# Performance work log

Measured on AMD Instinct MI355X. Metric: run time of the kernel, lower is better.

The kernel has to match this reference:

```python
import jax, jax.numpy as jnp
import numpy as np

N_LAYERS = 24
HID = 512
HEADS = 16
HEAD_DIM = HID // HEADS
CAP = 2048
VOCAB = 1025
EOS = 1024
FF = 2048
PE_LEN = 4096
EPS = 1e-5


def setup_inputs() -> dict:
    key = jax.random.key(0)
    ks = jax.random.split(key, 24)
    g = lambda k, shp, s=0.05: jax.random.normal(k, shp, jnp.float32) * s
    return {
        'last_token': jax.random.randint(ks[0], (1, 1), 0, 1024, dtype=jnp.int32),
        'position_index': jax.random.randint(ks[1], (1,), 0, 1024, dtype=jnp.int32),
        'cache_len': jax.random.randint(ks[2], (1,), 0, 1024, dtype=jnp.int32),
        'k_cache': g(ks[3], (N_LAYERS, 1, CAP, HID)),
        'v_cache': g(ks[4], (N_LAYERS, 1, CAP, HID)),
        'emb_table': g(ks[5], (VOCAB, HID)),
        'pe_table': g(ks[6], (PE_LEN, HID)),
        'x_scale': jnp.ones((1,), jnp.float32),
        'alpha': jnp.ones((1,), jnp.float32),
        'qkv_w_t': g(ks[7], (N_LAYERS, HID, 3 * HID)),
        'qkv_b': g(ks[8], (N_LAYERS, 3 * HID)),
        'out_w_t': g(ks[9], (N_LAYERS, HID, HID)),
        'out_b': g(ks[10], (N_LAYERS, HID)),
        'norm_w1': jnp.ones((N_LAYERS, HID), jnp.float32),
        'norm_b1': jnp.zeros((N_LAYERS, HID), jnp.float32),
        'norm_w2': jnp.ones((N_LAYERS, HID), jnp.float32),
        'norm_b2': jnp.zeros((N_LAYERS, HID), jnp.float32),
        'w1_t': g(ks[11], (N_LAYERS, HID, FF)),
        'b1': g(ks[12], (N_LAYERS, FF)),
        'w2_t': g(ks[13], (N_LAYERS, FF, HID)),
        'b2': g(ks[14], (N_LAYERS, HID)),
        'pred_w': g(ks[15], (VOCAB, HID)),
        'pred_b': g(ks[16], (VOCAB,)),
    }


def _layer_norm(x, w, b):
    mu = jnp.mean(x, axis=-1, keepdims=True)
    var = jnp.mean((x - mu) ** 2, axis=-1, keepdims=True)
    return (x - mu) * jax.lax.rsqrt(var + EPS) * w + b


def _decode_core(xy, cache_len, k_cache, v_cache, qkv_w_t, qkv_b, out_w_t, out_b,
                 norm_w1, norm_b1, norm_w2, norm_b2, w1_t, b1, w2_t, b2):
    B, Q, _ = xy.shape  # [1, 1, HID]
    clen = cache_len.astype(jnp.int32).reshape(1)
    next_len = clen + Q
    positions = jnp.arange(CAP)
    write_mask = (positions == clen)[None, :, None]           # [1, CAP, 1]
    valid = (positions < next_len)[None, :, None]             # [1, CAP, 1]
    inv_attn = (positions >= next_len)[None, None, None, :]   # [1, 1, 1, CAP]

    def layer(x, p):
        qw, qb, ow, ob, nw1, nb1, nw2, nb2, W1, B1, W2, B2, kc, vc = p
        qkv = x @ qw + qb                       # [B, Q, 3*HID]
        q, k, v = jnp.split(qkv, 3, axis=-1)
        # one-hot slot write + zero invalid tail (faithful to _update_cache_slot/_zero_invalid_cache_tail)
        kc = jnp.where(valid, jnp.where(write_mask, k, kc), 0.0)
        vc = jnp.where(valid, jnp.where(write_mask, v, vc), 0.0)
        qh = q.reshape(B, Q, HEADS, HEAD_DIM).transpose(0, 2, 1, 3)
        kh = kc.reshape(B, CAP, HEADS, HEAD_DIM).transpose(0, 2, 1, 3)
        vh = vc.reshape(B, CAP, HEADS, HEAD_DIM).transpose(0, 2, 1, 3)
        scores = jnp.einsum('bhqd,bhkd->bhqk', qh, kh) / jnp.sqrt(jnp.float32(HEAD_DIM))
        scores = jnp.where(inv_attn, jnp.float32(-1e30), scores)
        attn = jax.nn.softmax(scores, axis=-1)
        o = jnp.einsum('bhqk,bhkd->bhqd', attn, vh).transpose(0, 2, 1, 3).reshape(B, Q, HID)
        o = o @ ow + ob
        x = _layer_norm(x + o, nw1, nb1)
        h = jax.nn.relu(x @ W1 + B1) @ W2 + B2
        x = _layer_norm(x + h, nw2, nb2)
        return x, (kc, vc)

    x, (k_out, v_out) = jax.lax.scan(
        layer, xy,
        (qkv_w_t, qkv_b, out_w_t, out_b, norm_w1, norm_b1, norm_w2, norm_b2,
         w1_t, b1, w2_t, b2, k_cache, v_cache))
    return x, k_out, v_out, next_len


def reference(last_token, position_index, cache_len, k_cache, v_cache,
              emb_table, pe_table, x_scale, alpha,
              qkv_w_t, qkv_b, out_w_t, out_b,
              norm_w1, norm_b1, norm_w2, norm_b2,
              w1_t, b1, w2_t, b2, pred_w, pred_b):
    y_emb = emb_table[last_token]                              # [B, Q, HID]
    pos = pe_table[position_index.astype(jnp.int32)][None]     # [1, Q, HID]
    xy = y_emb * x_scale[0] + alpha[0] * pos
    x, k_out, v_out, next_len = _decode_core(
        xy, cache_len, k_cache, v_cache, qkv_w_t, qkv_b, out_w_t, out_b,
        norm_w1, norm_b1, norm_w2, norm_b2, w1_t, b1, w2_t, b2)
    logits = x[:, -1] @ pred_w.T + pred_b                      # [B, VOCAB]
    sampled = jnp.argmax(logits, axis=-1, keepdims=True).astype(jnp.int32)
    eos = (sampled.reshape(-1) == EOS).astype(jnp.int32)
    next_pos = position_index.astype(jnp.int32).reshape(1) + 1
    return (logits, sampled, eos, next_len, next_pos, k_out, v_out)
```

## Files before the change

### kernel.cpp

```cpp
#include <hip/hip_runtime.h>
#include <math.h>

#define NL     24
#define HIDDEN 512
#define H3     1536
#define HD     32
#define CAPCTX 2048
#define FFD    2048
#define NVOCAB 1025
#define GRID   256
#define NT     256
#define EPSLN  1e-5f
#define ISQ    0.17677669529663687f

__device__ __forceinline__ float gld(const float* p){ return __hip_atomic_load(p, __ATOMIC_RELAXED, __HIP_MEMORY_SCOPE_AGENT); }
__device__ __forceinline__ void  gst(float* p, float v){ __hip_atomic_store(p, v, __ATOMIC_RELAXED, __HIP_MEMORY_SCOPE_AGENT); }
__device__ __forceinline__ int   ild(const int* p){ return __hip_atomic_load(p, __ATOMIC_RELAXED, __HIP_MEMORY_SCOPE_AGENT); }
__device__ __forceinline__ void  ist(int* p, int v){ __hip_atomic_store(p, v, __ATOMIC_RELAXED, __HIP_MEMORY_SCOPE_AGENT); }

__device__ __forceinline__ void done_add(int* ctr, int tid){
  __syncthreads();
  if (tid == 0) __hip_atomic_fetch_add(ctr, 1, __ATOMIC_RELAXED, __HIP_MEMORY_SCOPE_AGENT);
}
__device__ __forceinline__ void waitge1(const int* c, int tgt){
  if (threadIdx.x == 0){
    int g = 0;
    while (__hip_atomic_load(c, __ATOMIC_RELAXED, __HIP_MEMORY_SCOPE_AGENT) < tgt){
      if (++g > (1<<25)) break;
    }
  }
  __syncthreads();
}
__device__ __forceinline__ void waitgeN(const int* base, int n, int tgt){
  if ((int)threadIdx.x < n){
    const int* c = base + threadIdx.x*16;
    int g = 0;
    while (__hip_atomic_load(c, __ATOMIC_RELAXED, __HIP_MEMORY_SCOPE_AGENT) < tgt){
      if (++g > (1<<25)) break;
    }
  }
  __syncthreads();
}
#define PIN() asm volatile("" ::: "memory")

#define KVF(kb)   ((kb)*16)
#define HEADC(h)  ((64+(h))*16)
#define FF1G(g)   ((80+(g))*16)
#define PRED_C    (88*16)
#define SLINE(par,h) ((90 + (par)*16 + (h))*16)

struct LdsF { float xn[HIDDEN]; float red[16*17]; float r8[8]; float s16[16]; float h16[16]; };
struct LdsAt{ float xn[HIDDEN]; float q[HD]; float e[128]; float v[128*33]; float red[288]; float r8[8]; float o32[HD]; };
union  Lds  { LdsF f; LdsAt a; };

__device__ __forceinline__ void bsum2(float &a, float &bb, float* lds8, int tid){
  #pragma unroll
  for (int o=32;o;o>>=1){ a += __shfl_down(a,o); bb += __shfl_down(bb,o); }
  __syncthreads();
  if ((tid&63)==0){ int w=tid>>6; lds8[w]=a; lds8[4+w]=bb; }
  __syncthreads();
  a  = lds8[0]+lds8[1]+lds8[2]+lds8[3];
  bb = lds8[4]+lds8[5]+lds8[6]+lds8[7];
  __syncthreads();
}

template<int K>
__device__ __forceinline__ float dotred(const float* w, const float* xn, float* red, int tid){
  const int c = tid & 15, s = tid >> 4;
  float a = 0.f;
  #pragma unroll
  for (int k=0;k<K;k++) a += xn[s + 16*k] * w[k];
  red[s*17 + c] = a;
  __syncthreads();
  float d = 0.f;
  if (s == 0){
    #pragma unroll
    for (int k=0;k<16;k++) d += red[k*17 + c];
  }
  __syncthreads();
  return d;
}

__device__ __forceinline__ void kvcopy(int idx, int T, int l, int clen,
    const float* __restrict__ KC, const float* __restrict__ VC,
    float* KO, float* VO, int tid){
  const int t7 = tid & 127, halfr = tid >> 7;
  const float4 z4 = make_float4(0.f,0.f,0.f,0.f);
  for (int r0 = idx*2; r0 < 4096; r0 += 2*T){
    int r = r0 + halfr;
    int p = r & 2047, isv = r >> 11;
    if (p != clen){
      float4* dst = (float4*)((isv ? VO : KO) + ((size_t)l*CAPCTX + p)*HIDDEN);
      if (p < clen){
        const float4* src = (const float4*)((isv ? VC : KC) + ((size_t)l*CAPCTX + p)*HIDDEN);
        dst[t7] = src[t7];
      } else {
        dst[t7] = z4;
      }
    }
  }
}

__global__ __launch_bounds__(NT, 1)
void t2s_decode(const int* __restrict__ LT, const int* __restrict__ PI, const int* __restrict__ CL,
                const float* __restrict__ KC, const float* __restrict__ VC,
                const float* __restrict__ EMB, const float* __restrict__ PE,
                const float* __restrict__ XSc, const float* __restrict__ ALp,
                const float* __restrict__ QKVW, const float* __restrict__ QKVB,
                const float* __restrict__ OUTW, const float* __restrict__ OUTB,
                const float* __restrict__ NW1, const float* __restrict__ NB1,
                const float* __restrict__ NW2, const float* __restrict__ NB2,
                const float* __restrict__ W1, const float* __restrict__ B1,
                const float* __restrict__ W2, const float* __restrict__ B2,
                const float* __restrict__ PW, const float* __restrict__ PB,
                float* __restrict__ OUT, float* __restrict__ WS)
{
  __shared__ Lds L;
  const int b = blockIdx.x, tid = threadIdx.x;

  int* C = (int*)WS;
  float* F   = WS + 2048;
  float* wop = F;
  float* wf2 = F + 16384;
  float* wx  = F + 24576;
  float* wx1 = F + 25088;
  float* wkv = F + 25600;

  float* KO = OUT + 1029;
  float* VO = KO + (size_t)NL*CAPCTX*HIDDEN;

  const int token = LT[0], posi = PI[0], clen = CL[0], nlen = clen + 1;
  const int nch = (nlen + 127) >> 7;
  const int T_copy = 128 + 16*(8 - nch);

  if (b >= 128){
    const int t = b - 128, h = t & 15, ci = t >> 4;
    const int cstar = clen >> 7;

    if (ci >= nch){
      const int idx = 128 + (ci - nch)*16 + h;
      for (int l=0;l<NL;l++) kvcopy(idx, T_copy, l, clen, KC, VC, KO, VO, tid);
    } else {
      const int c = tid & 31, s5 = tid >> 5;
      const int pl = tid >> 1, half = tid & 1, dbase = half << 4;
      const int p = (ci << 7) + pl;
      const bool validp = (p < nlen);
      const bool isnew  = validp && (p == clen);

      for (int l=0;l<NL;l++){
        const int par = l & 1;
        float pfQ[64];
        {
          const float* Wq = QKVW + (size_t)l*HIDDEN*H3 + (size_t)s5*H3 + h*HD + c;
          #pragma unroll
          for (int k=0;k<64;k++) pfQ[k] = Wq[(size_t)(k*8)*H3];
        }
        float qb = QKVB[(size_t)l*H3 + h*HD + c];
        float pfO[64];
        {
          const float* Wo = OUTW + (size_t)l*HIDDEN*HIDDEN + (size_t)(h*HD)*HIDDEN + tid;
          #pragma unroll
          for (int d=0;d<32;d++){ pfO[d] = Wo[(size_t)d*HIDDEN]; pfO[32+d] = Wo[(size_t)d*HIDDEN + 256]; }
        }
        float kbuf[16], vbuf[16];
        if (validp && !isnew){
          const size_t rowoff = ((size_t)l*CAPCTX + p)*HIDDEN + h*HD + dbase;
          const float4* sk = (const float4*)(KC + rowoff);
          const float4* sv = (const float4*)(VC + rowoff);
          #pragma unroll
          for (int k4=0;k4<4;k4++){
            float4 a = sk[k4];
            kbuf[4*k4]=a.x; kbuf[4*k4+1]=a.y; kbuf[4*k4+2]=a.z; kbuf[4*k4+3]=a.w;
            float4 cc = sv[k4];
            vbuf[4*k4]=cc.x; vbuf[4*k4+1]=cc.y; vbuf[4*k4+2]=cc.z; vbuf[4*k4+3]=cc.w;
          }
        }
        float lnb[2]={0,0}, lnw[2]={0,0}, lnn[2]={0,0};
        if (l > 0){
          #pragma unroll
          for (int r=0;r<2;r++){
            int i = tid + r*NT;
            lnb[r] = B2[(size_t)(l-1)*HIDDEN + i];
            lnw[r] = NW2[(size_t)(l-1)*HIDDEN + i];
            lnn[r] = NB2[(size_t)(l-1)*HIDDEN + i];
          }
        }
        PIN();

        if (l > 0) waitgeN(C + FF1G(0), 8, 16*l);

        float xn0, xn1;
        if (l == 0){
          float xs = XSc[0], al = ALp[0];
          xn0 = EMB[(size_t)token*HIDDEN + tid]*xs       + al*PE[(size_t)posi*HIDDEN + tid];
          xn1 = EMB[(size_t)token*HIDDEN + tid + 256]*xs + al*PE[(size_t)posi*HIDDEN + tid + 256];
        } else {
          float t0 = gld(&wx1[tid]) + lnb[0];
          float t1 = gld(&wx1[tid+256]) + lnb[1];
          const float* f2p = wf2 + (par^1)*4096;
          #pragma unroll
          for (int rg=0; rg<8; rg++){
            t0 += gld(&f2p[rg*512 + tid]);
            t1 += gld(&f2p[rg*512 + tid + 256]);
          }
          float s1 = t0 + t1, s2 = t0*t0 + t1*t1;
          bsum2(s1, s2, L.a.r8, tid);
          float mu = s1*(1.f/HIDDEN), rstd = rsqrtf(s2*(1.f/HIDDEN)-mu*mu+EPSLN);
          xn0 = (t0-mu)*rstd*lnw[0] + lnn[0];
          xn1 = (t1-mu)*rstd*lnw[1] + lnn[1];
        }
        L.a.xn[tid] = xn0; L.a.xn[tid+256] = xn1;
        if (b == 128){ gst(&wx[tid], xn0); gst(&wx[tid+256], xn1); }
        __syncthreads();

        {
          float qa = 0.f;
          #pragma unroll
          for (int k=0;k<64;k++) qa += L.a.xn[s5 + 8*k] * pfQ[k];
          L.a.red[s5*33 + c] = qa;
          __syncthreads();
          if (tid < 32){
            float qs = 0.f;
            #pragma unroll
            for (int k=0;k<8;k++) qs += L.a.red[k*33 + tid];
            L.a.q[tid] = (qs + qb) * ISQ;
          }
          __syncthreads();
        }

        if (ci == cstar){
          if (tid < 4){
            int kb = (tid>>1)*32 + 2*h + (tid&1);
            const int* fl = C + KVF(kb);
            int g = 0;
            while (ild(fl) < l+1){ if (++g > (1<<25)) break; }
          }
          __syncthreads();
        }

        float e = 0.f;
        if (validp){
          if (isnew){
            #pragma unroll
            for (int k=0;k<16;k++){
              kbuf[k] = gld(&wkv[h*HD + dbase + k]);
              vbuf[k] = gld(&wkv[512 + h*HD + dbase + k]);
            }
          }
          float dot = 0.f;
          #pragma unroll
          for (int k=0;k<16;k++) dot += kbuf[k] * L.a.q[dbase + k];
          dot += __shfl_xor(dot, 1);
          e = expf(dot);
        } else {
          #pragma unroll
          for (int k=0;k<16;k++) vbuf[k] = 0.f;
        }
        if (half == 0) L.a.e[pl] = validp ? e : 0.f;
        #pragma unroll
        for (int k=0;k<16;k++) L.a.v[pl*33 + dbase + k] = vbuf[k];
        __syncthreads();

        float se = (tid < 128) ? L.a.e[tid] : 0.f;
        #pragma unroll
        for (int o=32;o;o>>=1) se += __shfl_xor(se, o);
        if ((tid&63)==0) L.a.r8[tid>>6] = se;
        __syncthreads();
        const float S_ci = L.a.r8[0]+L.a.r8[1]+L.a.r8[2]+L.a.r8[3];

        {
          const int d = tid & 31, grp = tid >> 5;
          float oacc = 0.f;
          #pragma unroll
          for (int q2=0;q2<16;q2++){ int pp = (grp<<4) + q2; oacc += L.a.e[pp] * L.a.v[pp*33 + d]; }
          L.a.red[tid] = oacc;
          __syncthreads();
          if (tid < 32){
            float o8 = 0.f;
            #pragma unroll
            for (int g=0; g<8; g++) o8 += L.a.red[tid + (g<<5)];
            L.a.o32[tid] = o8;
          }
          if (tid == 0) unsafeAtomicAdd((float*)(C + SLINE(par,h)), S_ci);
          __syncthreads();
        }

        {
          float a0 = 0.f, a1 = 0.f;
          #pragma unroll
          for (int d=0; d<32; d++){ a0 += L.a.o32[d]*pfO[d]; a1 += L.a.o32[d]*pfO[32+d]; }
          unsafeAtomicAdd(&wop[par*8192 + h*512 + tid], a0);
          unsafeAtomicAdd(&wop[par*8192 + h*512 + 256 + tid], a1);
        }
        done_add(&C[HEADC(h)], tid);
      }
    }
    return;
  }

  {
    const int f = b, rgrp = f >> 4;
    const bool iskv = (f < 64);
    const int mat = f >> 5;
    const int c0  = (f & 31) << 4;

    for (int l=0;l<NL;l++){
      const int par = l & 1;
      float pfKV[32]; float pfKb = 0.f;
      float lnb[2]={0,0}, lnw[2]={0,0}, lnn[2]={0,0};
      if (iskv){
        const float* Wk = QKVW + (size_t)l*HIDDEN*H3 + (size_t)(tid>>4)*H3 + HIDDEN + mat*HIDDEN + c0 + (tid&15);
        #pragma unroll
        for (int k=0;k<32;k++) pfKV[k] = Wk[(size_t)(k*16)*H3];
        pfKb = QKVB[(size_t)l*H3 + HIDDEN + mat*HIDDEN + c0 + (tid&15)];
        if (l > 0){
          #pragma unroll
          for (int r=0;r<2;r++){
            int i = tid + r*NT;
            lnb[r] = B2[(size_t)(l-1)*HIDDEN + i];
            lnw[r] = NW2[(size_t)(l-1)*HIDDEN + i];
            lnn[r] = NB2[(size_t)(l-1)*HIDDEN + i];
          }
        }
      }
      float pfF1[32];
      {
        const float* W1p = W1 + (size_t)l*HIDDEN*FFD + (size_t)(tid>>4)*FFD + f*16 + (tid&15);
        #pragma unroll
        for (int k=0;k<32;k++) pfF1[k] = W1p[(size_t)(k*16)*FFD];
      }
      float pfF2[32];
      {
        const float* W2p = W2 + (size_t)l*FFD*HIDDEN + (size_t)(f*16)*HIDDEN + tid;
        #pragma unroll
        for (int cc=0;cc<16;cc++){ pfF2[cc] = W2p[(size_t)cc*HIDDEN]; pfF2[16+cc] = W2p[(size_t)cc*HIDDEN + 256]; }
      }
      float pfOB[2], pfW1n[2], pfB1n[2];
      #pragma unroll
      for (int r=0;r<2;r++){
        int i = tid + r*NT;
        pfOB[r]  = OUTB[(size_t)l*HIDDEN + i];
        pfW1n[r] = NW1[(size_t)l*HIDDEN + i];
        pfB1n[r] = NB1[(size_t)l*HIDDEN + i];
      }
      float pfB1f = B1[(size_t)l*FFD + f*16 + (tid&15)];
      PIN();

      if (iskv){
        if (l > 0){
          waitgeN(C + FF1G(0), 8, 16*l);
          float t0 = gld(&wx1[tid]) + lnb[0];
          float t1 = gld(&wx1[tid+256]) + lnb[1];
          const float* f2p = wf2 + (par^1)*4096;
          #pragma unroll
          for (int rg=0; rg<8; rg++){
            t0 += gld(&f2p[rg*512 + tid]);
            t1 += gld(&f2p[rg*512 + tid + 256]);
          }
          float s1 = t0 + t1, s2 = t0*t0 + t1*t1;
          bsum2(s1, s2, L.f.r8, tid);
          float mu = s1*(1.f/HIDDEN), rstd = rsqrtf(s2*(1.f/HIDDEN)-mu*mu+EPSLN);
          L.f.xn[tid]     = (t0-mu)*rstd*lnw[0] + lnn[0];
          L.f.xn[tid+256] = (t1-mu)*rstd*lnw[1] + lnn[1];
        } else {
          float xs = XSc[0], al = ALp[0];
          L.f.xn[tid]     = EMB[(size_t)token*HIDDEN + tid]*xs       + al*PE[(size_t)posi*HIDDEN + tid];
          L.f.xn[tid+256] = EMB[(size_t)token*HIDDEN + tid + 256]*xs + al*PE[(size_t)posi*HIDDEN + tid + 256];
        }
        __syncthreads();
        float dsum = dotred<32>(pfKV, L.f.xn, L.f.red, tid);
        if (tid < 16){
          int j = c0 + tid;
          float val = dsum + pfKb;
          gst(&wkv[mat*HIDDEN + j], val);
          float* dst = (mat ? VO : KO) + ((size_t)l*CAPCTX + clen)*HIDDEN + j;
          *dst = val;
        }
        __syncthreads();
        if (tid == 0) ist(&C[KVF(f)], l+1);
      }

      kvcopy(f, T_copy, l, clen, KC, VC, KO, VO, tid);

      waitgeN(C + HEADC(0), 16, nch*(l+1));

      if (tid < 64) gst(&wop[(par^1)*8192 + (f>>3)*512 + (f&7)*64 + tid], 0.f);
      if (tid < 32) gst(&wf2[(par^1)*4096 + f*32 + tid], 0.f);
      if (f < 16 && tid == 0) gst((float*)(C + SLINE(par^1, f)), 0.f);

      if (tid < 16) L.f.s16[tid] = 1.f / gld((const float*)(C + SLINE(par, tid)));
      __syncthreads();
      float t0 = gld(&wx[tid]) + pfOB[0];
      float t1 = gld(&wx[tid+256]) + pfOB[1];
      #pragma unroll
      for (int h2=0; h2<16; h2++){
        float is = L.f.s16[h2];
        t0 += gld(&wop[par*8192 + h2*512 + tid]) * is;
        t1 += gld(&wop[par*8192 + h2*512 + tid + 256]) * is;
      }
      float s1 = t0 + t1, s2 = t0*t0 + t1*t1;
      bsum2(s1, s2, L.f.r8, tid);
      float mu = s1*(1.f/HIDDEN), rstd = rsqrtf(s2*(1.f/HIDDEN)-mu*mu+EPSLN);
      float xn0 = (t0-mu)*rstd*pfW1n[0] + pfB1n[0];
      float xn1 = (t1-mu)*rstd*pfW1n[1] + pfB1n[1];
      L.f.xn[tid] = xn0; L.f.xn[tid+256] = xn1;
      if (f == 0){ gst(&wx1[tid], xn0); gst(&wx1[tid+256], xn1); }
      __syncthreads();

      float dsum = dotred<32>(pfF1, L.f.xn, L.f.red, tid);
      if (tid < 16) L.f.h16[tid] = fmaxf(dsum + pfB1f, 0.f);
      __syncthreads();
      float a0 = 0.f, a1 = 0.f;
      #pragma unroll
      for (int cc=0; cc<16; cc++){ float hv = L.f.h16[cc]; a0 += hv*pfF2[cc]; a1 += hv*pfF2[16+cc]; }
      unsafeAtomicAdd(&wf2[par*4096 + rgrp*512 + tid], a0);
      unsafeAtomicAdd(&wf2[par*4096 + rgrp*512 + 256 + tid], a1);
      done_add(&C[FF1G(rgrp)], tid);
    }

    if (f < 65){
      const int v0 = f << 4;
      const int nrows = (f == 64) ? 1 : 16;
      const int rr = tid >> 4, s2l = tid & 15;
      float pfP[32]; float pfPb = 0.f;
      if (rr < nrows){
        const float* row = PW + (size_t)(v0+rr)*HIDDEN;
        #pragma unroll
        for (int mm=0; mm<32; mm++) pfP[mm] = row[s2l + (mm<<4)];
        pfPb = PB[v0+rr];
      }
      float lnb[2], lnw[2], lnn[2];
      #pragma unroll
      for (int r=0;r<2;r++){
        int i = tid + r*NT;
        lnb[r] = B2[(size_t)(NL-1)*HIDDEN + i];
        lnw[r] = NW2[(size_t)(NL-1)*HIDDEN + i];
        lnn[r] = NB2[(size_t)(NL-1)*HIDDEN + i];
      }
      PIN();
      waitgeN(C + FF1G(0), 8, 16*NL);
      float t0 = gld(&wx1[tid]) + lnb[0];
      float t1 = gld(&wx1[tid+256]) + lnb[1];
      const float* f2p = wf2 + 4096;
      #pragma unroll
      for (int rg=0; rg<8; rg++){
        t0 += gld(&f2p[rg*512 + tid]);
        t1 += gld(&f2p[rg*512 + tid + 256]);
      }
      float s1 = t0 + t1, s2 = t0*t0 + t1*t1;
      bsum2(s1, s2, L.f.r8, tid);
      float mu = s1*(1.f/HIDDEN), rstd = rsqrtf(s2*(1.f/HIDDEN)-mu*mu+EPSLN);
      L.f.xn[tid]     = (t0-mu)*rstd*lnw[0] + lnn[0];
      L.f.xn[tid+256] = (t1-mu)*rstd*lnw[1] + lnn[1];
      __syncthreads();
      if (rr < nrows){
        float acc = 0.f;
        #pragma unroll
        for (int mm=0; mm<32; mm++) acc += L.f.xn[s2l + (mm<<4)] * pfP[mm];
        #pragma unroll
        for (int o=1;o<16;o<<=1) acc += __shfl_xor(acc, o);
        if (s2l == 0) gst(&OUT[v0+rr], acc + pfPb);
      }
      done_add(&C[PRED_C], tid);
    }

    if (b == 0){
      waitge1(&C[PRED_C], 65);
      float bv = -3.0e38f; int bi = 0;
      for (int v=tid; v<NVOCAB; v+=NT){
        float x = gld(&OUT[v]);
        if (x > bv){ bv = x; bi = v; }
      }
      L.f.xn[tid] = bv;
      ((int*)&L.f.xn[256])[tid] = bi;
      __syncthreads();
      for (int step=128; step; step>>=1){
        if (tid < step){
          float ov2 = L.f.xn[tid+step]; int oi = ((int*)&L.f.xn[256])[tid+step];
          float mv  = L.f.xn[tid];      int mi = ((int*)&L.f.xn[256])[tid];
          if (ov2 > mv || (ov2 == mv && oi < mi)){ L.f.xn[tid]=ov2; ((int*)&L.f.xn[256])[tid]=oi; }
        }
        __syncthreads();
      }
      if (tid == 0){
        int bi0 = ((int*)&L.f.xn[256])[0];
        OUT[NVOCAB]   = (float)bi0;
        OUT[NVOCAB+1] = (bi0 == 1024) ? 1.f : 0.f;
        OUT[NVOCAB+2] = (float)nlen;
        OUT[NVOCAB+3] = (float)(posi + 1);
      }
    }
  }
}

extern "C" void kernel_launch(void* const* d_in, const int* in_sizes, int n_in,
                              void* d_out, int out_size, void* d_ws, size_t ws_size,
                              hipStream_t stream) {
  (void)in_sizes; (void)n_in; (void)out_size; (void)ws_size;
  hipMemsetAsync(d_ws, 0, 8192 + 65536 + 32768, stream);
  t2s_decode<<<GRID, NT, 0, stream>>>(
    (const int*)d_in[0], (const int*)d_in[1], (const int*)d_in[2],
    (const float*)d_in[3], (const float*)d_in[4],
    (const float*)d_in[5], (const float*)d_in[6],
    (const float*)d_in[7], (const float*)d_in[8],
    (const float*)d_in[9], (const float*)d_in[10],
    (const float*)d_in[11], (const float*)d_in[12],
    (const float*)d_in[13], (const float*)d_in[14],
    (const float*)d_in[15], (const float*)d_in[16],
    (const float*)d_in[17], (const float*)d_in[18],
    (const float*)d_in[19], (const float*)d_in[20],
    (const float*)d_in[21], (const float*)d_in[22],
    (float*)d_out, (float*)d_ws);
}
```

Baseline: 340.8 us.

## Compute new K/V inside attention blocks instead of separate FF blocks

The K and V projections for the new token move out of the 64 FF-side blocks, which had to publish them through workspace and flags. The attention blocks owning the chunk that holds the current position now compute them directly alongside Q and keep them in LDS. This removes a cross-block flag wait and global round trip on the critical path each layer, and also drops the LN recomputation in those FF blocks. In exchange those attention blocks do three times the projection work and hold more registers. Softmax exp switches to the fast intrinsic.

After: 344.7 us. No clear change (+1.2%).

```diff
diff --git a/kernel.cpp b/kernel.cpp
--- a/kernel.cpp
+++ b/kernel.cpp
@@ -16,7 +16,6 @@
 __device__ __forceinline__ float gld(const float* p){ return __hip_atomic_load(p, __ATOMIC_RELAXED, __HIP_MEMORY_SCOPE_AGENT); }
 __device__ __forceinline__ void  gst(float* p, float v){ __hip_atomic_store(p, v, __ATOMIC_RELAXED, __HIP_MEMORY_SCOPE_AGENT); }
 __device__ __forceinline__ int   ild(const int* p){ return __hip_atomic_load(p, __ATOMIC_RELAXED, __HIP_MEMORY_SCOPE_AGENT); }
-__device__ __forceinline__ void  ist(int* p, int v){ __hip_atomic_store(p, v, __ATOMIC_RELAXED, __HIP_MEMORY_SCOPE_AGENT); }
 
 __device__ __forceinline__ void done_add(int* ctr, int tid){
   __syncthreads();
@@ -43,14 +42,13 @@
 }
 #define PIN() asm volatile("" ::: "memory")
 
-#define KVF(kb)   ((kb)*16)
-#define HEADC(h)  ((64+(h))*16)
-#define FF1G(g)   ((80+(g))*16)
-#define PRED_C    (88*16)
-#define SLINE(par,h) ((90 + (par)*16 + (h))*16)
+#define HEADC(h)  ((h)*16)
+#define FF1G(g)   ((16+(g))*16)
+#define PRED_C    (24*16)
+#define SLINE(par,h) ((26 + (par)*16 + (h))*16)
 
 struct LdsF { float xn[HIDDEN]; float red[16*17]; float r8[8]; float s16[16]; float h16[16]; };
-struct LdsAt{ float xn[HIDDEN]; float q[HD]; float e[128]; float v[128*33]; float red[288]; float r8[8]; float o32[HD]; };
+struct LdsAt{ float xn[HIDDEN]; float q[HD]; float kv[64]; float e[128]; float v[128*33]; float red[792]; float r8[8]; float o32[HD]; };
 union  Lds  { LdsF f; LdsAt a; };
 
 __device__ __forceinline__ void bsum2(float &a, float &bb, float* lds8, int tid){
@@ -62,23 +60,6 @@
   a  = lds8[0]+lds8[1]+lds8[2]+lds8[3];
   bb = lds8[4]+lds8[5]+lds8[6]+lds8[7];
   __syncthreads();
-}
-
-template<int K>
-__device__ __forceinline__ float dotred(const float* w, const float* xn, float* red, int tid){
-  const int c = tid & 15, s = tid >> 4;
-  float a = 0.f;
-  #pragma unroll
-  for (int k=0;k<K;k++) a += xn[s + 16*k] * w[k];
-  red[s*17 + c] = a;
-  __syncthreads();
-  float d = 0.f;
-  if (s == 0){
-    #pragma unroll
-    for (int k=0;k<16;k++) d += red[k*17 + c];
-  }
-  __syncthreads();
-  return d;
 }
 
 __device__ __forceinline__ void kvcopy(int idx, int T, int l, int clen,
@@ -119,12 +100,11 @@
   const int b = blockIdx.x, tid = threadIdx.x;
 
   int* C = (int*)WS;
-  float* F   = WS + 2048;
+  float* F   = WS + 1024;
   float* wop = F;
   float* wf2 = F + 16384;
   float* wx  = F + 24576;
   float* wx1 = F + 25088;
-  float* wkv = F + 25600;
 
   float* KO = OUT + 1029;
   float* VO = KO + (size_t)NL*CAPCTX*HIDDEN;
@@ -146,16 +126,26 @@
       const int p = (ci << 7) + pl;
       const bool validp = (p < nlen);
       const bool isnew  = validp && (p == clen);
+      const bool iscstar = (ci == cstar);
 
       for (int l=0;l<NL;l++){
         const int par = l & 1;
-        float pfQ[64];
+        float pfQ[64], pfK[64], pfV[64];
+        float qb, kb = 0.f, vb = 0.f;
         {
           const float* Wq = QKVW + (size_t)l*HIDDEN*H3 + (size_t)s5*H3 + h*HD + c;
           #pragma unroll
           for (int k=0;k<64;k++) pfQ[k] = Wq[(size_t)(k*8)*H3];
-        }
-        float qb = QKVB[(size_t)l*H3 + h*HD + c];
+          qb = QKVB[(size_t)l*H3 + h*HD + c];
+          if (iscstar){
+            const float* Wk = QKVW + (size_t)l*HIDDEN*H3 + (size_t)s5*H3 + HIDDEN + h*HD + c;
+            const float* Wv = Wk + HIDDEN;
+            #pragma unroll
+            for (int k=0;k<64;k++){ pfK[k] = Wk[(size_t)(k*8)*H3]; pfV[k] = Wv[(size_t)(k*8)*H3]; }
+            kb = QKVB[(size_t)l*H3 + HIDDEN + h*HD + c];
+            vb = QKVB[(size_t)l*H3 + 2*HIDDEN + h*HD + c];
+          }
+        }
         float pfO[64];
         {
           const float* Wo = OUTW + (size_t)l*HIDDEN*HIDDEN + (size_t)(h*HD)*HIDDEN + tid;
@@ -214,26 +204,30 @@
         __syncthreads();
 
         {
-          float qa = 0.f;
-          #pragma unroll
-          for (int k=0;k<64;k++) qa += L.a.xn[s5 + 8*k] * pfQ[k];
+          float qa = 0.f, ka = 0.f, va = 0.f;
+          #pragma unroll
+          for (int k=0;k<64;k++){
+            float xv = L.a.xn[s5 + 8*k];
+            qa += xv * pfQ[k];
+            if (iscstar){ ka += xv * pfK[k]; va += xv * pfV[k]; }
+          }
           L.a.red[s5*33 + c] = qa;
+          if (iscstar){ L.a.red[264 + s5*33 + c] = ka; L.a.red[528 + s5*33 + c] = va; }
           __syncthreads();
           if (tid < 32){
             float qs = 0.f;
             #pragma unroll
             for (int k=0;k<8;k++) qs += L.a.red[k*33 + tid];
             L.a.q[tid] = (qs + qb) * ISQ;
-          }
-          __syncthreads();
-        }
-
-        if (ci == cstar){
-          if (tid < 4){
-            int kb = (tid>>1)*32 + 2*h + (tid&1);
-            const int* fl = C + KVF(kb);
-            int g = 0;
-            while (ild(fl) < l+1){ if (++g > (1<<25)) break; }
+            if (iscstar){
+              float ks = 0.f, vs = 0.f;
+              #pragma unroll
+              for (int k=0;k<8;k++){ ks += L.a.red[264 + k*33 + tid]; vs += L.a.red[528 + k*33 + tid]; }
+              ks += kb; vs += vb;
+              L.a.kv[tid] = ks; L.a.kv[32+tid] = vs;
+              KO[((size_t)l*CAPCTX + clen)*HIDDEN + h*HD + tid] = ks;
+              VO[((size_t)l*CAPCTX + clen)*HIDDEN + h*HD + tid] = vs;
+            }
           }
           __syncthreads();
         }
@@ -242,16 +236,13 @@
         if (validp){
           if (isnew){
             #pragma unroll
-            for (int k=0;k<16;k++){
-              kbuf[k] = gld(&wkv[h*HD + dbase + k]);
-              vbuf[k] = gld(&wkv[512 + h*HD + dbase + k]);
-            }
+            for (int k=0;k<16;k++){ kbuf[k] = L.a.kv[dbase+k]; vbuf[k] = L.a.kv[32+dbase+k]; }
           }
           float dot = 0.f;
           #pragma unroll
           for (int k=0;k<16;k++) dot += kbuf[k] * L.a.q[dbase + k];
           dot += __shfl_xor(dot, 1);
-          e = expf(dot);
+          e = __expf(dot);
         } else {
           #pragma unroll
           for (int k=0;k<16;k++) vbuf[k] = 0.f;
@@ -260,13 +251,6 @@
         #pragma unroll
         for (int k=0;k<16;k++) L.a.v[pl*33 + dbase + k] = vbuf[k];
         __syncthreads();
-
-        float se = (tid < 128) ? L.a.e[tid] : 0.f;
-        #pragma unroll
-        for (int o=32;o;o>>=1) se += __shfl_xor(se, o);
-        if ((tid&63)==0) L.a.r8[tid>>6] = se;
-        __syncthreads();
-        const float S_ci = L.a.r8[0]+L.a.r8[1]+L.a.r8[2]+L.a.r8[3];
 
         {
           const int d = tid & 31, grp = tid >> 5;
@@ -274,14 +258,21 @@
           #pragma unroll
           for (int q2=0;q2<16;q2++){ int pp = (grp<<4) + q2; oacc += L.a.e[pp] * L.a.v[pp*33 + d]; }
           L.a.red[tid] = oacc;
+          float se = (tid < 128) ? L.a.e[tid] : 0.f;
+          #pragma unroll
+          for (int o=32;o;o>>=1) se += __shfl_xor(se, o);
+          if ((tid&63)==0) L.a.r8[tid>>6] = se;
           __syncthreads();
+          if (tid == 0){
+            float S_ci = L.a.r8[0]+L.a.r8[1]+L.a.r8[2]+L.a.r8[3];
+            unsafeAtomicAdd((float*)(C + SLINE(par,h)), S_ci);
+          }
           if (tid < 32){
             float o8 = 0.f;
             #pragma unroll
             for (int g=0; g<8; g++) o8 += L.a.red[tid + (g<<5)];
             L.a.o32[tid] = o8;
           }
-          if (tid == 0) unsafeAtomicAdd((float*)(C + SLINE(par,h)), S_ci);
           __syncthreads();
         }
 
@@ -300,29 +291,9 @@
 
   {
     const int f = b, rgrp = f >> 4;
-    const bool iskv = (f < 64);
-    const int mat = f >> 5;
-    const int c0  = (f & 31) << 4;
 
     for (int l=0;l<NL;l++){
       const int par = l & 1;
-      float pfKV[32]; float pfKb = 0.f;
-      float lnb[2]={0,0}, lnw[2]={0,0}, lnn[2]={0,0};
-      if (iskv){
-        const float* Wk = QKVW + (size_t)l*HIDDEN*H3 + (size_t)(tid>>4)*H3 + HIDDEN + mat*HIDDEN + c0 + (tid&15);
-        #pragma unroll
-        for (int k=0;k<32;k++) pfKV[k] = Wk[(size_t)(k*16)*H3];
-        pfKb = QKVB[(size_t)l*H3 + HIDDEN + mat*HIDDEN + c0 + (tid&15)];
-        if (l > 0){
-          #pragma unroll
-          for (int r=0;r<2;r++){
-            int i = tid + r*NT;
-            lnb[r] = B2[(size_t)(l-1)*HIDDEN + i];
-            lnw[r] = NW2[(size_t)(l-1)*HIDDEN + i];
-            lnn[r] = NB2[(size_t)(l-1)*HIDDEN + i];
-          }
-        }
-      }
       float pfF1[32];
       {
         const float* W1p = W1 + (size_t)l*HIDDEN*FFD + (size_t)(tid>>4)*FFD + f*16 + (tid&15);
@@ -345,40 +316,6 @@
       }
       float pfB1f = B1[(size_t)l*FFD + f*16 + (tid&15)];
       PIN();
-
-      if (iskv){
-        if (l > 0){
-          waitgeN(C + FF1G(0), 8, 16*l);
-          float t0 = gld(&wx1[tid]) + lnb[0];
-          float t1 = gld(&wx1[tid+256]) + lnb[1];
-          const float* f2p = wf2 + (par^1)*4096;
-          #pragma unroll
-          for (int rg=0; rg<8; rg++){
-            t0 += gld(&f2p[rg*512 + tid]);
-            t1 += gld(&f2p[rg*512 + tid + 256]);
-          }
-          float s1 = t0 + t1, s2 = t0*t0 + t1*t1;
-          bsum2(s1, s2, L.f.r8, tid);
-          float mu = s1*(1.f/HIDDEN), rstd = rsqrtf(s2*(1.f/HIDDEN)-mu*mu+EPSLN);
-          L.f.xn[tid]     = (t0-mu)*rstd*lnw[0] + lnn[0];
-          L.f.xn[tid+256] = (t1-mu)*rstd*lnw[1] + lnn[1];
-        } else {
-          float xs = XSc[0], al = ALp[0];
-          L.f.xn[tid]     = EMB[(size_t)token*HIDDEN + tid]*xs       + al*PE[(size_t)posi*HIDDEN + tid];
-          L.f.xn[tid+256] = EMB[(size_t)token*HIDDEN + tid + 256]*xs + al*PE[(size_t)posi*HIDDEN + tid + 256];
-        }
-        __syncthreads();
-        float dsum = dotred<32>(pfKV, L.f.xn, L.f.red, tid);
-        if (tid < 16){
-          int j = c0 + tid;
-          float val = dsum + pfKb;
-          gst(&wkv[mat*HIDDEN + j], val);
-          float* dst = (mat ? VO : KO) + ((size_t)l*CAPCTX + clen)*HIDDEN + j;
-          *dst = val;
-        }
-        __syncthreads();
-        if (tid == 0) ist(&C[KVF(f)], l+1);
-      }
 
       kvcopy(f, T_copy, l, clen, KC, VC, KO, VO, tid);
 
@@ -407,9 +344,21 @@
       if (f == 0){ gst(&wx1[tid], xn0); gst(&wx1[tid+256], xn1); }
       __syncthreads();
 
-      float dsum = dotred<32>(pfF1, L.f.xn, L.f.red, tid);
-      if (tid < 16) L.f.h16[tid] = fmaxf(dsum + pfB1f, 0.f);
-      __syncthreads();
+      {
+        const int cc = tid & 15, s = tid >> 4;
+        float a = 0.f;
+        #pragma unroll
+        for (int k=0;k<32;k++) a += L.f.xn[s + 16*k] * pfF1[k];
+        L.f.red[s*17 + cc] = a;
+        __syncthreads();
+        if (tid < 16){
+          float dd = 0.f;
+          #pragma unroll
+          for (int k=0;k<16;k++) dd += L.f.red[k*17 + tid];
+          L.f.h16[tid] = fmaxf(dd + pfB1f, 0.f);
+        }
+        __syncthreads();
+      }
       float a0 = 0.f, a1 = 0.f;
       #pragma unroll
       for (int cc=0; cc<16; cc++){ float hv = L.f.h16[cc]; a0 += hv*pfF2[cc]; a1 += hv*pfF2[16+cc]; }
@@ -497,7 +446,7 @@
                               void* d_out, int out_size, void* d_ws, size_t ws_size,
                               hipStream_t stream) {
   (void)in_sizes; (void)n_in; (void)out_size; (void)ws_size;
-  hipMemsetAsync(d_ws, 0, 8192 + 65536 + 32768, stream);
+  hipMemsetAsync(d_ws, 0, 4096 + 65536 + 32768, stream);
   t2s_decode<<<GRID, NT, 0, stream>>>(
     (const int*)d_in[0], (const int*)d_in[1], (const int*)d_in[2],
     (const float*)d_in[3], (const float*)d_in[4],
```

## Fold per-head softmax normalisation into last-arriving attention block and shrink FFN reduction groups

Applied to the files above, without the earlier changes.

The last attention block to finish each head now normalises that head's partial output by the softmax sum and adds it into a single combined buffer, then signals one FFN-ready counter. FFN blocks wait on that one counter instead of polling sixteen head counters and summing sixteen scaled partials. FFN output partials are cut from eight to four groups, so fewer slots are read and zeroed, and the KV cache copy is spread across all attention blocks with a fixed stride. It also uses the fast __expf, which risks small accuracy differences, and adds a serial tail step on the last block of each head.

Result: slower. 373.7 us (+9.7%).

```diff
diff --git a/kernel.cpp b/kernel.cpp
--- a/kernel.cpp
+++ b/kernel.cpp
@@ -46,10 +46,11 @@
 #define KVF(kb)   ((kb)*16)
 #define HEADC(h)  ((64+(h))*16)
 #define FF1G(g)   ((80+(g))*16)
-#define PRED_C    (88*16)
-#define SLINE(par,h) ((90 + (par)*16 + (h))*16)
-
-struct LdsF { float xn[HIDDEN]; float red[16*17]; float r8[8]; float s16[16]; float h16[16]; };
+#define FFNRDY    (84*16)
+#define PRED_C    (85*16)
+#define SLINE(par,h) ((88+(par)*16+(h))*16)
+
+struct LdsF { float xn[HIDDEN]; float red[16*17]; float r8[8]; float h16[16]; };
 struct LdsAt{ float xn[HIDDEN]; float q[HD]; float e[128]; float v[128*33]; float red[288]; float r8[8]; float o32[HD]; };
 union  Lds  { LdsF f; LdsAt a; };
 
@@ -81,12 +82,12 @@
   return d;
 }
 
-__device__ __forceinline__ void kvcopy(int idx, int T, int l, int clen,
+__device__ __forceinline__ void kvcopy(int idx, int l, int clen,
     const float* __restrict__ KC, const float* __restrict__ VC,
     float* KO, float* VO, int tid){
   const int t7 = tid & 127, halfr = tid >> 7;
   const float4 z4 = make_float4(0.f,0.f,0.f,0.f);
-  for (int r0 = idx*2; r0 < 4096; r0 += 2*T){
+  for (int r0 = idx*2; r0 < 4096; r0 += 512){
     int r = r0 + halfr;
     int p = r & 2047, isv = r >> 11;
     if (p != clen){
@@ -116,36 +117,37 @@
                 float* __restrict__ OUT, float* __restrict__ WS)
 {
   __shared__ Lds L;
+  __shared__ int lastflag;
   const int b = blockIdx.x, tid = threadIdx.x;
 
   int* C = (int*)WS;
   float* F   = WS + 2048;
-  float* wop = F;
-  float* wf2 = F + 16384;
-  float* wx  = F + 24576;
-  float* wx1 = F + 25088;
-  float* wkv = F + 25600;
+  float* wos = F;
+  float* wfs = F + 1024;
+  float* wop = F + 5120;
+  float* wx  = F + 21504;
+  float* wx1 = F + 22016;
+  float* wkv = F + 22528;
 
   float* KO = OUT + 1029;
   float* VO = KO + (size_t)NL*CAPCTX*HIDDEN;
 
   const int token = LT[0], posi = PI[0], clen = CL[0], nlen = clen + 1;
   const int nch = (nlen + 127) >> 7;
-  const int T_copy = 128 + 16*(8 - nch);
 
   if (b >= 128){
     const int t = b - 128, h = t & 15, ci = t >> 4;
     const int cstar = clen >> 7;
 
     if (ci >= nch){
-      const int idx = 128 + (ci - nch)*16 + h;
-      for (int l=0;l<NL;l++) kvcopy(idx, T_copy, l, clen, KC, VC, KO, VO, tid);
+      for (int l=0;l<NL;l++) kvcopy(b, l, clen, KC, VC, KO, VO, tid);
     } else {
       const int c = tid & 31, s5 = tid >> 5;
       const int pl = tid >> 1, half = tid & 1, dbase = half << 4;
       const int p = (ci << 7) + pl;
       const bool validp = (p < nlen);
       const bool isnew  = validp && (p == clen);
+      const bool iscstar = (ci == cstar);
 
       for (int l=0;l<NL;l++){
         const int par = l & 1;
@@ -187,7 +189,7 @@
         }
         PIN();
 
-        if (l > 0) waitgeN(C + FF1G(0), 8, 16*l);
+        if (l > 0) waitgeN(C + FF1G(0), 4, 32*l);
 
         float xn0, xn1;
         if (l == 0){
@@ -197,11 +199,11 @@
         } else {
           float t0 = gld(&wx1[tid]) + lnb[0];
           float t1 = gld(&wx1[tid+256]) + lnb[1];
-          const float* f2p = wf2 + (par^1)*4096;
-          #pragma unroll
-          for (int rg=0; rg<8; rg++){
-            t0 += gld(&f2p[rg*512 + tid]);
-            t1 += gld(&f2p[rg*512 + tid + 256]);
+          const float* f2p = wfs + (par^1)*2048;
+          #pragma unroll
+          for (int g=0; g<4; g++){
+            t0 += gld(&f2p[g*512 + tid]);
+            t1 += gld(&f2p[g*512 + tid + 256]);
           }
           float s1 = t0 + t1, s2 = t0*t0 + t1*t1;
           bsum2(s1, s2, L.a.r8, tid);
@@ -228,7 +230,7 @@
           __syncthreads();
         }
 
-        if (ci == cstar){
+        if (iscstar){
           if (tid < 4){
             int kb = (tid>>1)*32 + 2*h + (tid&1);
             const int* fl = C + KVF(kb);
@@ -251,7 +253,7 @@
           #pragma unroll
           for (int k=0;k<16;k++) dot += kbuf[k] * L.a.q[dbase + k];
           dot += __shfl_xor(dot, 1);
-          e = expf(dot);
+          e = __expf(dot);
         } else {
           #pragma unroll
           for (int k=0;k<16;k++) vbuf[k] = 0.f;
@@ -260,13 +262,6 @@
         #pragma unroll
         for (int k=0;k<16;k++) L.a.v[pl*33 + dbase + k] = vbuf[k];
         __syncthreads();
-
-        float se = (tid < 128) ? L.a.e[tid] : 0.f;
-        #pragma unroll
-        for (int o=32;o;o>>=1) se += __shfl_xor(se, o);
-        if ((tid&63)==0) L.a.r8[tid>>6] = se;
-        __syncthreads();
-        const float S_ci = L.a.r8[0]+L.a.r8[1]+L.a.r8[2]+L.a.r8[3];
 
         {
           const int d = tid & 31, grp = tid >> 5;
@@ -274,14 +269,21 @@
           #pragma unroll
           for (int q2=0;q2<16;q2++){ int pp = (grp<<4) + q2; oacc += L.a.e[pp] * L.a.v[pp*33 + d]; }
           L.a.red[tid] = oacc;
+          float se = (tid < 128) ? L.a.e[tid] : 0.f;
+          #pragma unroll
+          for (int o=32;o;o>>=1) se += __shfl_xor(se, o);
+          if ((tid&63)==0) L.a.r8[tid>>6] = se;
           __syncthreads();
+          if (tid == 0){
+            float S_ci = L.a.r8[0]+L.a.r8[1]+L.a.r8[2]+L.a.r8[3];
+            unsafeAtomicAdd((float*)(C + SLINE(par,h)), S_ci);
+          }
           if (tid < 32){
             float o8 = 0.f;
             #pragma unroll
             for (int g=0; g<8; g++) o8 += L.a.red[tid + (g<<5)];
             L.a.o32[tid] = o8;
           }
-          if (tid == 0) unsafeAtomicAdd((float*)(C + SLINE(par,h)), S_ci);
           __syncthreads();
         }
 
@@ -292,14 +294,31 @@
           unsafeAtomicAdd(&wop[par*8192 + h*512 + tid], a0);
           unsafeAtomicAdd(&wop[par*8192 + h*512 + 256 + tid], a1);
         }
-        done_add(&C[HEADC(h)], tid);
+
+        __syncthreads();
+        if (tid == 0){
+          int old = __hip_atomic_fetch_add(&C[HEADC(h)], 1, __ATOMIC_RELAXED, __HIP_MEMORY_SCOPE_AGENT);
+          lastflag = (old == nch*(l+1)-1) ? 1 : 0;
+        }
+        __syncthreads();
+        if (lastflag){
+          float inv = 1.f / gld((const float*)(C + SLINE(par,h)));
+          float v0 = gld(&wop[par*8192 + h*512 + tid]) * inv;
+          float v1 = gld(&wop[par*8192 + h*512 + 256 + tid]) * inv;
+          unsafeAtomicAdd(&wos[par*512 + tid], v0);
+          unsafeAtomicAdd(&wos[par*512 + 256 + tid], v1);
+          __syncthreads();
+          if (tid == 0) __hip_atomic_fetch_add(&C[FFNRDY], 1, __ATOMIC_RELAXED, __HIP_MEMORY_SCOPE_AGENT);
+        }
+
+        kvcopy(b, l, clen, KC, VC, KO, VO, tid);
       }
     }
     return;
   }
 
   {
-    const int f = b, rgrp = f >> 4;
+    const int f = b, g4 = f >> 5;
     const bool iskv = (f < 64);
     const int mat = f >> 5;
     const int c0  = (f & 31) << 4;
@@ -348,14 +367,14 @@
 
       if (iskv){
         if (l > 0){
-          waitgeN(C + FF1G(0), 8, 16*l);
+          waitgeN(C + FF1G(0), 4, 32*l);
           float t0 = gld(&wx1[tid]) + lnb[0];
           float t1 = gld(&wx1[tid+256]) + lnb[1];
-          const float* f2p = wf2 + (par^1)*4096;
-          #pragma unroll
-          for (int rg=0; rg<8; rg++){
-            t0 += gld(&f2p[rg*512 + tid]);
-            t1 += gld(&f2p[rg*512 + tid + 256]);
+          const float* f2p = wfs + (par^1)*2048;
+          #pragma unroll
+          for (int g=0; g<4; g++){
+            t0 += gld(&f2p[g*512 + tid]);
+            t1 += gld(&f2p[g*512 + tid + 256]);
           }
           float s1 = t0 + t1, s2 = t0*t0 + t1*t1;
           bsum2(s1, s2, L.f.r8, tid);
@@ -380,24 +399,17 @@
         if (tid == 0) ist(&C[KVF(f)], l+1);
       }
 
-      kvcopy(f, T_copy, l, clen, KC, VC, KO, VO, tid);
-
-      waitgeN(C + HEADC(0), 16, nch*(l+1));
-
-      if (tid < 64) gst(&wop[(par^1)*8192 + (f>>3)*512 + (f&7)*64 + tid], 0.f);
-      if (tid < 32) gst(&wf2[(par^1)*4096 + f*32 + tid], 0.f);
+      kvcopy(f, l, clen, KC, VC, KO, VO, tid);
+
+      waitge1(&C[FFNRDY], 16*(l+1));
+
+      if (tid < 64) gst(&wop[(par^1)*8192 + f*64 + tid], 0.f);
+      if (tid < 16) gst(&wfs[(par^1)*2048 + f*16 + tid], 0.f);
+      if (tid < 4)  gst(&wos[(par^1)*512 + f*4 + tid], 0.f);
       if (f < 16 && tid == 0) gst((float*)(C + SLINE(par^1, f)), 0.f);
 
-      if (tid < 16) L.f.s16[tid] = 1.f / gld((const float*)(C + SLINE(par, tid)));
-      __syncthreads();
-      float t0 = gld(&wx[tid]) + pfOB[0];
-      float t1 = gld(&wx[tid+256]) + pfOB[1];
-      #pragma unroll
-      for (int h2=0; h2<16; h2++){
-        float is = L.f.s16[h2];
-        t0 += gld(&wop[par*8192 + h2*512 + tid]) * is;
-        t1 += gld(&wop[par*8192 + h2*512 + tid + 256]) * is;
-      }
+      float t0 = gld(&wx[tid]) + pfOB[0] + gld(&wos[par*512 + tid]);
+      float t1 = gld(&wx[tid+256]) + pfOB[1] + gld(&wos[par*512 + 256 + tid]);
       float s1 = t0 + t1, s2 = t0*t0 + t1*t1;
       bsum2(s1, s2, L.f.r8, tid);
       float mu = s1*(1.f/HIDDEN), rstd = rsqrtf(s2*(1.f/HIDDEN)-mu*mu+EPSLN);
@@ -407,15 +419,27 @@
       if (f == 0){ gst(&wx1[tid], xn0); gst(&wx1[tid+256], xn1); }
       __syncthreads();
 
-      float dsum = dotred<32>(pfF1, L.f.xn, L.f.red, tid);
-      if (tid < 16) L.f.h16[tid] = fmaxf(dsum + pfB1f, 0.f);
-      __syncthreads();
+      {
+        const int cc = tid & 15, s = tid >> 4;
+        float a = 0.f;
+        #pragma unroll
+        for (int k=0;k<32;k++) a += L.f.xn[s + 16*k] * pfF1[k];
+        L.f.red[s*17 + cc] = a;
+        __syncthreads();
+        if (tid < 16){
+          float dd = 0.f;
+          #pragma unroll
+          for (int k=0;k<16;k++) dd += L.f.red[k*17 + tid];
+          L.f.h16[tid] = fmaxf(dd + pfB1f, 0.f);
+        }
+        __syncthreads();
+      }
       float a0 = 0.f, a1 = 0.f;
       #pragma unroll
       for (int cc=0; cc<16; cc++){ float hv = L.f.h16[cc]; a0 += hv*pfF2[cc]; a1 += hv*pfF2[16+cc]; }
-      unsafeAtomicAdd(&wf2[par*4096 + rgrp*512 + tid], a0);
-      unsafeAtomicAdd(&wf2[par*4096 + rgrp*512 + 256 + tid], a1);
-      done_add(&C[FF1G(rgrp)], tid);
+      unsafeAtomicAdd(&wfs[par*2048 + g4*512 + tid], a0);
+      unsafeAtomicAdd(&wfs[par*2048 + g4*512 + 256 + tid], a1);
+      done_add(&C[FF1G(g4)], tid);
     }
 
     if (f < 65){
@@ -438,14 +462,14 @@
         lnn[r] = NB2[(size_t)(NL-1)*HIDDEN + i];
       }
       PIN();
-      waitgeN(C + FF1G(0), 8, 16*NL);
+      waitgeN(C + FF1G(0), 4, 32*NL);
       float t0 = gld(&wx1[tid]) + lnb[0];
       float t1 = gld(&wx1[tid+256]) + lnb[1];
-      const float* f2p = wf2 + 4096;
+      const float* f2p = wfs + 2048;
       #pragma unroll
-      for (int rg=0; rg<8; rg++){
-        t0 += gld(&f2p[rg*512 + tid]);
-        t1 += gld(&f2p[rg*512 + tid + 256]);
+      for (int g=0; g<4; g++){
+        t0 += gld(&f2p[g*512 + tid]);
+        t1 += gld(&f2p[g*512 + tid + 256]);
       }
       float s1 = t0 + t1, s2 = t0*t0 + t1*t1;
       bsum2(s1, s2, L.f.r8, tid);
@@ -497,7 +521,7 @@
                               void* d_out, int out_size, void* d_ws, size_t ws_size,
                               hipStream_t stream) {
   (void)in_sizes; (void)n_in; (void)out_size; (void)ws_size;
-  hipMemsetAsync(d_ws, 0, 8192 + 65536 + 32768, stream);
+  hipMemsetAsync(d_ws, 0, 8192 + 21504*4, stream);
   t2s_decode<<<GRID, NT, 0, stream>>>(
     (const int*)d_in[0], (const int*)d_in[1], (const int*)d_in[2],
     (const float*)d_in[3], (const float*)d_in[4],
```
